# Kernel optimization log

Measured on AMD Instinct MI355X. Metric: run time of the kernel, lower is better.

## Reference

```python
import jax, jax.numpy as jnp
import numpy as np

N_NODES = 100000
N_EDGES = 1600000
N_GRAPHS = 2048
HID = 64
IN_F = 14
N_CLS = 2
EPS = 1e-5


def _gcn_conv(x, row, col, w_edge, W, b, n_nodes):
    # PyG GCNConv with add_self_loops=True, normalize=True.
    xw = x @ W  # [N, out]
    # degree on target nodes, self-loop contributes weight 1
    deg = jnp.zeros((n_nodes,), x.dtype).at[col].add(w_edge) + 1.0
    dinv = deg ** -0.5
    norm = dinv[row] * w_edge * dinv[col]  # [E]
    out = jnp.zeros_like(xw).at[col].add(norm[:, None] * xw[row])
    out = out + (dinv * dinv)[:, None] * xw  # self-loop term
    return out + b


def _bn_relu(x, gamma, beta):
    mean = jnp.mean(x, axis=0)
    var = jnp.var(x, axis=0)  # biased, as PyTorch BN training normalization
    y = gamma * (x - mean) * jax.lax.rsqrt(var + EPS) + beta
    return jax.nn.relu(y)


def setup_inputs() -> dict:
    key = jax.random.key(0)
    ks = jax.random.split(key, 8)
    x = jax.random.normal(ks[0], (N_NODES, IN_F), dtype=jnp.float32)
    edge_index = jax.random.randint(ks[1], (2, N_EDGES), 0, N_NODES, dtype=jnp.int64)
    batch = jnp.sort(jax.random.randint(ks[2], (N_NODES,), 0, N_GRAPHS, dtype=jnp.int64))
    edge_weight = jnp.ones((N_EDGES,), dtype=jnp.float32)
    def lin(k, fi, fo):
        s = 1.0 / np.sqrt(fi)
        kw, kb = jax.random.split(k)
        return (jax.random.uniform(kw, (fi, fo), jnp.float32, -s, s),
                jax.random.uniform(kb, (fo,), jnp.float32, -s, s))
    W1, b1 = lin(ks[3], IN_F, HID)
    W2, b2 = lin(ks[4], HID, HID)
    W3, b3 = lin(ks[5], HID, HID)
    fcW, fcb = lin(ks[6], HID, N_CLS)
    g = jnp.ones((HID,), jnp.float32)
    z = jnp.zeros((HID,), jnp.float32)
    return {
        "x": x, "edge_index": edge_index, "batch": batch, "edge_weight": edge_weight,
        "W1": W1, "b1": b1, "W2": W2, "b2": b2, "W3": W3, "b3": b3,
        "g1": g, "bt1": z, "g2": g, "bt2": z, "g3": g, "bt3": z,
        "fcW": fcW, "fcb": fcb,
    }


def reference(x, edge_index, batch, edge_weight, W1, b1, W2, b2, W3, b3,
              g1, bt1, g2, bt2, g3, bt3, fcW, fcb):
    row, col = edge_index[0], edge_index[1]
    n = x.shape[0]
    h = _bn_relu(_gcn_conv(x, row, col, edge_weight, W1, b1, n), g1, bt1)
    h = _bn_relu(_gcn_conv(h, row, col, edge_weight, W2, b2, n), g2, bt2)
    h = _bn_relu(_gcn_conv(h, row, col, edge_weight, W3, b3, n), g3, bt3)
    node_embs = h  # dropout p=0 is identity
    graph_emb = jax.ops.segment_sum(node_embs, batch, num_segments=N_GRAPHS)
    out = graph_emb @ fcW + fcb
    return (out, node_embs, graph_emb)
```

## Files before the change

### kernel.cpp

```cpp
#include <hip/hip_runtime.h>

#define N_NODES 100000
#define N_EDGES 1600000
#define N_GRAPHS 2048
#define HID 64
#define IN_F 14
#define N_CLS 2
#define EPS 1e-5f

typedef _Float16 half_t;
typedef _Float16 half8 __attribute__((ext_vector_type(8)));
typedef float f32x4 __attribute__((ext_vector_type(4)));

#define GSTRIDE ((size_t)N_NODES * 16)

__global__ __launch_bounds__(256) void hist_rank_kernel(const int* __restrict__ col,
                                                        const float* __restrict__ w,
                                                        unsigned long long* __restrict__ packed,
                                                        int* __restrict__ rank, int E) {
    int stride = gridDim.x * blockDim.x;
    for (int e = blockIdx.x * blockDim.x + threadIdx.x; e < E; e += stride) {
        int c = col[e];
        unsigned int fx = __float2uint_rn(w[e] * 65536.0f);
        unsigned long long old =
            atomicAdd(&packed[c], ((unsigned long long)fx << 32) | 1ull);
        rank[e] = (int)(old & 0xffffffffull);
    }
}

__global__ __launch_bounds__(256) void dinv_from_packed(const unsigned long long* __restrict__ packed,
                                                        float* __restrict__ dinv, int n) {
    int i = blockIdx.x * blockDim.x + threadIdx.x;
    if (i < n) {
        float wsum = (float)(packed[i] >> 32) * (1.0f / 65536.0f);
        dinv[i] = rsqrtf(1.0f + wsum);
    }
}


__global__ __launch_bounds__(256) void blocksum1024_kernel(const unsigned long long* __restrict__ packed,
                                                           int* __restrict__ bsum, int n) {
    __shared__ int ls[256];
    int base = blockIdx.x * 1024 + threadIdx.x * 4;
    int s = 0;
#pragma unroll
    for (int k = 0; k < 4; k++) {
        int i = base + k;
        if (i < n) s += (int)(packed[i] & 0xffffffffull);
    }
    ls[threadIdx.x] = s;
    __syncthreads();
    for (int off = 128; off > 0; off >>= 1) {
        if (threadIdx.x < off) ls[threadIdx.x] += ls[threadIdx.x + off];
        __syncthreads();
    }
    if (threadIdx.x == 0) bsum[blockIdx.x] = ls[0];
}

__global__ __launch_bounds__(512) void topscan_kernel(int* __restrict__ bsum, int nb) {
    __shared__ int ls[512];
    int t = threadIdx.x;
    int v = (t < nb) ? bsum[t] : 0;
    ls[t] = v;
    __syncthreads();
    for (int off = 1; off < 512; off <<= 1) {
        int x = ls[t];
        if (t >= off) x += ls[t - off];
        __syncthreads();
        ls[t] = x;
        __syncthreads();
    }
    if (t < nb) bsum[t] = ls[t] - v;
}

__global__ __launch_bounds__(256) void blockscan1024_kernel(const unsigned long long* __restrict__ packed,
                                                            const int* __restrict__ bsum,
                                                            int* __restrict__ ptr, int n, int E) {
    __shared__ int ls[256];
    int base = blockIdx.x * 1024 + threadIdx.x * 4;
    int c[4];
    int s = 0;
#pragma unroll
    for (int k = 0; k < 4; k++) {
        int i = base + k;
        c[k] = (i < n) ? (int)(packed[i] & 0xffffffffull) : 0;
        s += c[k];
    }
    ls[threadIdx.x] = s;
    __syncthreads();
    for (int off = 1; off < 256; off <<= 1) {
        int x = ls[threadIdx.x];
        if (threadIdx.x >= off) x += ls[threadIdx.x - off];
        __syncthreads();
        ls[threadIdx.x] = x;
        __syncthreads();
    }
    int run = ls[threadIdx.x] - s + bsum[blockIdx.x];
#pragma unroll
    for (int k = 0; k < 4; k++) {
        int i = base + k;
        if (i < n) ptr[i] = run;
        run += c[k];
    }
    if (blockIdx.x == 0 && threadIdx.x == 0) ptr[n] = E;
}

__global__ __launch_bounds__(256) void permute_kernel(const int* __restrict__ row,
                                                      const int* __restrict__ col,
                                                      const float* __restrict__ w,
                                                      const float* __restrict__ dinv,
                                                      const int* __restrict__ ptr,
                                                      const int* __restrict__ rank,
                                                      unsigned int* __restrict__ edges, int E) {
    int stride = gridDim.x * blockDim.x;
    for (int e = blockIdx.x * blockDim.x + threadIdx.x; e < E; e += stride) {
        int r = row[e], c = col[e];
        int pos = ptr[c] + rank[e];
        float nrm = dinv[r] * w[e] * dinv[c];
        unsigned int nb = __float_as_uint(nrm);
        unsigned int n15 = (nb + 0x8000u) >> 16;
        if (n15 > 0x7fffu) n15 = 0x7fffu;
        edges[pos] = ((unsigned int)r << 15) | n15;
    }
}


template <int K>
__global__ __launch_bounds__(256) void gemm_kernel(const float* __restrict__ h,
                                                   const float* __restrict__ W,
                                                   half_t* __restrict__ xw, int n_nodes) {
    int f = threadIdx.x & 63;
    float wcol[K];
#pragma unroll
    for (int k = 0; k < K; k++) wcol[k] = W[k * HID + f];
    half_t* xg = xw + (size_t)(f >> 4) * GSTRIDE + (f & 15);
    int wave = (blockIdx.x * blockDim.x + threadIdx.x) >> 6;
    int nwaves = (gridDim.x * blockDim.x) >> 6;
    for (int n = wave; n < n_nodes; n += nwaves) {
        const float* hr = h + (size_t)n * K;
        float acc = 0.f;
#pragma unroll
        for (int k = 0; k < K; k++) acc += hr[k] * wcol[k];
        xg[(size_t)n * 16] = (half_t)acc;
    }
}

__global__ __launch_bounds__(256) void gemm_bn_mfma_kernel(const float* __restrict__ h,
                                                           const float* __restrict__ W,
                                                           const float* __restrict__ stats,
                                                           const float* __restrict__ gamma,
                                                           const float* __restrict__ beta,
                                                           half_t* __restrict__ xw, int n_nodes) {
    __shared__ float sc_s[HID], sh_s[HID];
    if (threadIdx.x < 64) {
        float mean = stats[threadIdx.x] * (1.0f / N_NODES);
        float var = stats[64 + threadIdx.x] * (1.0f / N_NODES) - mean * mean;
        float sc = gamma[threadIdx.x] * rsqrtf(var + EPS);
        sc_s[threadIdx.x] = sc;
        sh_s[threadIdx.x] = beta[threadIdx.x] - mean * sc;
    }
    __syncthreads();
    int lane = threadIdx.x & 63;
    int col16 = lane & 15;
    int quad = lane >> 4;

    float scA[2][8], shA[2][8];
#pragma unroll
    for (int kh = 0; kh < 2; kh++)
#pragma unroll
        for (int j = 0; j < 8; j++) {
            int k = kh * 32 + quad * 8 + j;
            scA[kh][j] = sc_s[k];
            shA[kh][j] = sh_s[k];
        }

    half8 bfrag[4][2];
#pragma unroll
    for (int t = 0; t < 4; t++)
#pragma unroll
        for (int kh = 0; kh < 2; kh++)
#pragma unroll
            for (int j = 0; j < 8; j++) {
                int k = kh * 32 + quad * 8 + j;
                bfrag[t][kh][j] = (half_t)W[k * HID + t * 16 + col16];
            }

    int wave = (blockIdx.x * blockDim.x + threadIdx.x) >> 6;
    int nwaves = (gridDim.x * blockDim.x) >> 6;
    int ntiles = n_nodes >> 4;
    for (int tIdx = wave; tIdx < ntiles; tIdx += nwaves) {
        int n0 = tIdx << 4;
        const float* hr = h + (size_t)(n0 + col16) * HID + quad * 8;
        half8 afrag[2];
#pragma unroll
        for (int kh = 0; kh < 2; kh++) {
            float4 p0 = *(const float4*)(hr + kh * 32);
            float4 p1 = *(const float4*)(hr + kh * 32 + 4);
            float fv[8] = {p0.x, p0.y, p0.z, p0.w, p1.x, p1.y, p1.z, p1.w};
#pragma unroll
            for (int j = 0; j < 8; j++) {
                float v = fv[j] * scA[kh][j] + shA[kh][j];
                afrag[kh][j] = (half_t)fmaxf(v, 0.f);
            }
        }
        f32x4 acc[4];
#pragma unroll
        for (int t = 0; t < 4; t++) {
            f32x4 z = {0.f, 0.f, 0.f, 0.f};
            acc[t] = __builtin_amdgcn_mfma_f32_16x16x32_f16(afrag[0], bfrag[t][0], z, 0, 0, 0);
            acc[t] = __builtin_amdgcn_mfma_f32_16x16x32_f16(afrag[1], bfrag[t][1], acc[t], 0, 0, 0);
        }
#pragma unroll
        for (int t = 0; t < 4; t++) {
            half_t* xg = xw + (size_t)t * GSTRIDE;
#pragma unroll
            for (int r = 0; r < 4; r++) {
                int rowi = n0 + quad * 4 + r;
                xg[(size_t)rowi * 16 + col16] = (half_t)acc[t][r];
            }
        }
    }
}

__global__ __launch_bounds__(256) void gather_stats_kernel(const int* __restrict__ ptr,
                                                           const unsigned int* __restrict__ edges,
                                                           const half_t* __restrict__ xw,
                                                           const float* __restrict__ dinv,
                                                           const float* __restrict__ b,
                                                           float* __restrict__ h,
                                                           float* __restrict__ stats,
                                                           int n_nodes) {
    int g = (blockIdx.x & 7) >> 1;
    int grank = ((blockIdx.x >> 3) << 1) | (blockIdx.x & 1);
    int lane16 = threadIdx.x & 15;
    int quadLocal = threadIdx.x >> 4;
    int quadId = grank * 16 + quadLocal;
    int nquads = (gridDim.x >> 2) * 16;

    const half_t* xg = xw + (size_t)g * GSTRIDE;
    const char* xgb = (const char*)xg + lane16 * 2;
    int f = g * 16 + lane16;
    float bf = b[f];
    int base = ((threadIdx.x & 63) >> 4) * 16;

    float s = 0.f, s2 = 0.f;
    for (int n = quadId; n < n_nodes; n += nquads) {
        int beg = ptr[n];
        int c = ptr[n + 1] - beg;
        float a0 = 0.f, a1 = 0.f, a2 = 0.f, a3 = 0.f;
        for (int j0 = 0; j0 < c; j0 += 16) {
            int m = c - j0;
            if (m > 16) m = 16;
            int ev = 0;
            if (lane16 < m) ev = (int)edges[beg + j0 + lane16];
            int j = 0;
            for (; j + 4 <= m; j += 4) {
                unsigned int u0 = (unsigned int)__shfl(ev, base + j);
                unsigned int u1 = (unsigned int)__shfl(ev, base + j + 1);
                unsigned int u2 = (unsigned int)__shfl(ev, base + j + 2);
                unsigned int u3 = (unsigned int)__shfl(ev, base + j + 3);
                float w0 = __uint_as_float((u0 & 0x7fffu) << 16);
                float w1 = __uint_as_float((u1 & 0x7fffu) << 16);
                float w2 = __uint_as_float((u2 & 0x7fffu) << 16);
                float w3 = __uint_as_float((u3 & 0x7fffu) << 16);
                float x0 = (float)*(const half_t*)(xgb + ((size_t)(u0 >> 15) << 5));
                float x1 = (float)*(const half_t*)(xgb + ((size_t)(u1 >> 15) << 5));
                float x2 = (float)*(const half_t*)(xgb + ((size_t)(u2 >> 15) << 5));
                float x3 = (float)*(const half_t*)(xgb + ((size_t)(u3 >> 15) << 5));
                a0 += w0 * x0; a1 += w1 * x1; a2 += w2 * x2; a3 += w3 * x3;
            }
            if (j < m) {
                unsigned int u = (unsigned int)__shfl(ev, base + j);
                a1 += __uint_as_float((u & 0x7fffu) << 16) *
                      (float)*(const half_t*)(xgb + ((size_t)(u >> 15) << 5));
            }
            if (j + 1 < m) {
                unsigned int u = (unsigned int)__shfl(ev, base + j + 1);
                a2 += __uint_as_float((u & 0x7fffu) << 16) *
                      (float)*(const half_t*)(xgb + ((size_t)(u >> 15) << 5));
            }
            if (j + 2 < m) {
                unsigned int u = (unsigned int)__shfl(ev, base + j + 2);
                a3 += __uint_as_float((u & 0x7fffu) << 16) *
                      (float)*(const half_t*)(xgb + ((size_t)(u >> 15) << 5));
            }
        }
        float di = dinv[n];
        float v = ((a0 + a1) + (a2 + a3)) + di * di * (float)xg[(size_t)n * 16 + lane16] + bf;
        h[(size_t)n * HID + f] = v;
        s += v;
        s2 += v * v;
    }
    __shared__ float ls[256], ls2[256];
    ls[threadIdx.x] = s;
    ls2[threadIdx.x] = s2;
    __syncthreads();
    if (threadIdx.x < 16) {
        float a = 0.f, aa = 0.f;
#pragma unroll
        for (int k = 0; k < 16; k++) {
            a += ls[k * 16 + threadIdx.x];
            aa += ls2[k * 16 + threadIdx.x];
        }
        atomicAdd(&stats[g * 16 + threadIdx.x], a);
        atomicAdd(&stats[64 + g * 16 + threadIdx.x], aa);
    }
}

__global__ __launch_bounds__(256) void bn_relu_seg_kernel(float* __restrict__ h,
                                                          const float* __restrict__ stats,
                                                          const float* __restrict__ gamma,
                                                          const float* __restrict__ beta,
                                                          const int* __restrict__ batch,
                                                          float* __restrict__ gemb,
                                                          int n_nodes) {
    int g = blockIdx.x * blockDim.x + threadIdx.x;
    int f = g & 63;
    int wave = g >> 6;
    int nwaves = (gridDim.x * blockDim.x) >> 6;
    int chunk = (n_nodes + nwaves - 1) / nwaves;
    int n0 = wave * chunk;
    int n1 = n0 + chunk;
    if (n1 > n_nodes) n1 = n_nodes;
    if (n0 >= n_nodes) return;
    float mean = stats[f] * (1.0f / N_NODES);
    float var = stats[64 + f] * (1.0f / N_NODES) - mean * mean;
    float sc = gamma[f] * rsqrtf(var + EPS);
    float sh = beta[f] - mean * sc;
    int curg = batch[n0];
    float racc = 0.f;
    for (int n = n0; n < n1; n++) {
        int bg = batch[n];
        if (bg != curg) {
            atomicAdd(&gemb[(size_t)curg * HID + f], racc);
            racc = 0.f;
            curg = bg;
        }
        size_t idx = (size_t)n * HID + f;
        float v = h[idx] * sc + sh;
        v = fmaxf(v, 0.f);
        h[idx] = v;
        racc += v;
    }
    atomicAdd(&gemb[(size_t)curg * HID + f], racc);
}

__global__ __launch_bounds__(256) void final_kernel(const float* __restrict__ gemb,
                                                    const float* __restrict__ fcW,
                                                    const float* __restrict__ fcb,
                                                    float* __restrict__ out) {
    int g = blockIdx.x * blockDim.x + threadIdx.x;
    if (g >= N_GRAPHS * N_CLS) return;
    int gr = g >> 1, c = g & 1;
    float acc = fcb[c];
#pragma unroll
    for (int k = 0; k < HID; k++) acc += gemb[gr * HID + k] * fcW[k * N_CLS + c];
    out[g] = acc;
}


extern "C" void kernel_launch(void* const* d_in, const int* in_sizes, int n_in,
                              void* d_out, int out_size, void* d_ws, size_t ws_size,
                              hipStream_t stream) {
    const float* x    = (const float*)d_in[0];
    const int*   ei   = (const int*)d_in[1];
    const int*   batch= (const int*)d_in[2];
    const float* ew   = (const float*)d_in[3];
    const float* W1   = (const float*)d_in[4];
    const float* b1   = (const float*)d_in[5];
    const float* W2   = (const float*)d_in[6];
    const float* b2   = (const float*)d_in[7];
    const float* W3   = (const float*)d_in[8];
    const float* b3   = (const float*)d_in[9];
    const float* g1   = (const float*)d_in[10];
    const float* bt1  = (const float*)d_in[11];
    const float* g2   = (const float*)d_in[12];
    const float* bt2  = (const float*)d_in[13];
    const float* g3   = (const float*)d_in[14];
    const float* bt3  = (const float*)d_in[15];
    const float* fcW  = (const float*)d_in[16];
    const float* fcb  = (const float*)d_in[17];

    const int* row = ei;
    const int* col = ei + N_EDGES;

    float* out_head  = (float*)d_out;
    float* node_embs = out_head + N_GRAPHS * N_CLS;
    float* gemb      = node_embs + (size_t)N_NODES * HID;

    half_t* xwh  = (half_t*)d_ws;
    unsigned int* edges = (unsigned int*)(xwh + (size_t)N_NODES * HID);
    unsigned long long* packed = (unsigned long long*)(edges + N_EDGES);
    float* dinv  = (float*)(packed + N_NODES);
    float* stats = dinv + N_NODES;
    int*   ptr   = (int*)(stats + 128);
    int*   rank  = ptr + N_NODES + 1;
    int*   bsum  = rank + N_EDGES;

    const int B   = 256;
    const int gN  = (N_NODES + B - 1) / B;
    const int NBS = (N_NODES + 1023) / 1024;
    const int gGS = 1024;
    const int gGA = 2048;

    hipMemsetAsync(packed, 0, N_NODES * sizeof(unsigned long long), stream);
    hist_rank_kernel<<<gGS, B, 0, stream>>>(col, ew, packed, rank, N_EDGES);
    dinv_from_packed<<<gN, B, 0, stream>>>(packed, dinv, N_NODES);
    blocksum1024_kernel<<<NBS, B, 0, stream>>>(packed, bsum, N_NODES);
    topscan_kernel<<<1, 512, 0, stream>>>(bsum, NBS);
    blockscan1024_kernel<<<NBS, B, 0, stream>>>(packed, bsum, ptr, N_NODES, N_EDGES);
    permute_kernel<<<gGS, B, 0, stream>>>(row, col, ew, dinv, ptr, rank, edges, N_EDGES);

    float* h = node_embs;

    gemm_kernel<IN_F><<<gGS, B, 0, stream>>>(x, W1, xwh, N_NODES);
    hipMemsetAsync(stats, 0, 128 * sizeof(float), stream);
    gather_stats_kernel<<<gGA, B, 0, stream>>>(ptr, edges, xwh, dinv, b1, h, stats, N_NODES);

    gemm_bn_mfma_kernel<<<gGS, B, 0, stream>>>(h, W2, stats, g1, bt1, xwh, N_NODES);
    hipMemsetAsync(stats, 0, 128 * sizeof(float), stream);
    gather_stats_kernel<<<gGA, B, 0, stream>>>(ptr, edges, xwh, dinv, b2, h, stats, N_NODES);

    gemm_bn_mfma_kernel<<<gGS, B, 0, stream>>>(h, W3, stats, g2, bt2, xwh, N_NODES);
    hipMemsetAsync(stats, 0, 128 * sizeof(float), stream);
    gather_stats_kernel<<<gGA, B, 0, stream>>>(ptr, edges, xwh, dinv, b3, h, stats, N_NODES);

    hipMemsetAsync(gemb, 0, (size_t)N_GRAPHS * HID * sizeof(float), stream);
    bn_relu_seg_kernel<<<gGS, B, 0, stream>>>(h, stats, g3, bt3, batch, gemb, N_NODES);

    final_kernel<<<(N_GRAPHS * N_CLS + B - 1) / B, B, 0, stream>>>(gemb, fcW, fcb, out_head);
}
```

Measured before the change: 493.9 us.

## Replace global-atomic CSR build with two-pass bucketed counting sort

The CSR construction previously used per-edge 64-bit global atomics on per-node counters to get degrees and ranks, followed by a scan and a permute. It is replaced by a two-level radix-style sort: per-block shared-memory histograms over 512-node buckets, a scan, a scatter into bucket order, then a per-bucket kernel that does local counting, prefix sums, dinv computation and final placement. The goal is to avoid heavy global atomic contention and random rank traffic. In exchange it adds extra passes over 8-byte edge records and quantizes edge weights to 13 fractional bits, and it aliases the workspace buffers (EB over xwh, EA over edges). Edge order within a node is now nondeterministic.

New measurement: 440.4 us. 1.12x faster.

```diff
diff --git a/kernel.cpp b/kernel.cpp
--- a/kernel.cpp
+++ b/kernel.cpp
@@ -8,53 +8,41 @@
 #define N_CLS 2
 #define EPS 1e-5f
 
+#define BSHIFT 9
+#define NBUCK 196
+#define ABLOCKS 256
+#define CHUNK (N_EDGES / ABLOCKS)
+
 typedef _Float16 half_t;
 typedef _Float16 half8 __attribute__((ext_vector_type(8)));
 typedef float f32x4 __attribute__((ext_vector_type(4)));
 
 #define GSTRIDE ((size_t)N_NODES * 16)
 
-__global__ __launch_bounds__(256) void hist_rank_kernel(const int* __restrict__ col,
-                                                        const float* __restrict__ w,
-                                                        unsigned long long* __restrict__ packed,
-                                                        int* __restrict__ rank, int E) {
-    int stride = gridDim.x * blockDim.x;
-    for (int e = blockIdx.x * blockDim.x + threadIdx.x; e < E; e += stride) {
-        int c = col[e];
-        unsigned int fx = __float2uint_rn(w[e] * 65536.0f);
-        unsigned long long old =
-            atomicAdd(&packed[c], ((unsigned long long)fx << 32) | 1ull);
-        rank[e] = (int)(old & 0xffffffffull);
-    }
-}
-
-__global__ __launch_bounds__(256) void dinv_from_packed(const unsigned long long* __restrict__ packed,
-                                                        float* __restrict__ dinv, int n) {
-    int i = blockIdx.x * blockDim.x + threadIdx.x;
-    if (i < n) {
-        float wsum = (float)(packed[i] >> 32) * (1.0f / 65536.0f);
-        dinv[i] = rsqrtf(1.0f + wsum);
-    }
-}
-
-
-__global__ __launch_bounds__(256) void blocksum1024_kernel(const unsigned long long* __restrict__ packed,
-                                                           int* __restrict__ bsum, int n) {
+
+__global__ __launch_bounds__(256) void histA_kernel(const int* __restrict__ col,
+                                                    int* __restrict__ histG) {
+    __shared__ int hl[NBUCK];
+    for (int i = threadIdx.x; i < NBUCK; i += 256) hl[i] = 0;
+    __syncthreads();
+    int e0 = blockIdx.x * CHUNK;
+    for (int e = e0 + threadIdx.x; e < e0 + CHUNK; e += 256)
+        atomicAdd(&hl[col[e] >> BSHIFT], 1);
+    __syncthreads();
+    for (int i = threadIdx.x; i < NBUCK; i += 256)
+        histG[i * ABLOCKS + blockIdx.x] = hl[i];
+}
+
+__global__ __launch_bounds__(256) void scanS1_kernel(const int* __restrict__ histG,
+                                                     int* __restrict__ bsumA) {
     __shared__ int ls[256];
-    int base = blockIdx.x * 1024 + threadIdx.x * 4;
-    int s = 0;
-#pragma unroll
-    for (int k = 0; k < 4; k++) {
-        int i = base + k;
-        if (i < n) s += (int)(packed[i] & 0xffffffffull);
-    }
-    ls[threadIdx.x] = s;
+    ls[threadIdx.x] = histG[blockIdx.x * 256 + threadIdx.x];
     __syncthreads();
     for (int off = 128; off > 0; off >>= 1) {
         if (threadIdx.x < off) ls[threadIdx.x] += ls[threadIdx.x + off];
         __syncthreads();
     }
-    if (threadIdx.x == 0) bsum[blockIdx.x] = ls[0];
+    if (threadIdx.x == 0) bsumA[blockIdx.x] = ls[0];
 }
 
 __global__ __launch_bounds__(512) void topscan_kernel(int* __restrict__ bsum, int nb) {
@@ -73,20 +61,13 @@
     if (t < nb) bsum[t] = ls[t] - v;
 }
 
-__global__ __launch_bounds__(256) void blockscan1024_kernel(const unsigned long long* __restrict__ packed,
-                                                            const int* __restrict__ bsum,
-                                                            int* __restrict__ ptr, int n, int E) {
+__global__ __launch_bounds__(256) void scanS3_kernel(int* __restrict__ histG,
+                                                     const int* __restrict__ bsumA,
+                                                     int* __restrict__ ptr) {
     __shared__ int ls[256];
-    int base = blockIdx.x * 1024 + threadIdx.x * 4;
-    int c[4];
-    int s = 0;
-#pragma unroll
-    for (int k = 0; k < 4; k++) {
-        int i = base + k;
-        c[k] = (i < n) ? (int)(packed[i] & 0xffffffffull) : 0;
-        s += c[k];
-    }
-    ls[threadIdx.x] = s;
+    int idx = blockIdx.x * 256 + threadIdx.x;
+    int v = histG[idx];
+    ls[threadIdx.x] = v;
     __syncthreads();
     for (int off = 1; off < 256; off <<= 1) {
         int x = ls[threadIdx.x];
@@ -95,32 +76,92 @@
         ls[threadIdx.x] = x;
         __syncthreads();
     }
-    int run = ls[threadIdx.x] - s + bsum[blockIdx.x];
-#pragma unroll
-    for (int k = 0; k < 4; k++) {
-        int i = base + k;
-        if (i < n) ptr[i] = run;
-        run += c[k];
-    }
-    if (blockIdx.x == 0 && threadIdx.x == 0) ptr[n] = E;
-}
-
-__global__ __launch_bounds__(256) void permute_kernel(const int* __restrict__ row,
-                                                      const int* __restrict__ col,
-                                                      const float* __restrict__ w,
-                                                      const float* __restrict__ dinv,
-                                                      const int* __restrict__ ptr,
-                                                      const int* __restrict__ rank,
-                                                      unsigned int* __restrict__ edges, int E) {
+    histG[idx] = ls[threadIdx.x] - v + bsumA[blockIdx.x];
+    if (blockIdx.x == 0 && threadIdx.x == 0) ptr[N_NODES] = N_EDGES;
+}
+
+__global__ __launch_bounds__(256) void scatterA_kernel(const int* __restrict__ row,
+                                                       const int* __restrict__ col,
+                                                       const float* __restrict__ w,
+                                                       const int* __restrict__ histG,
+                                                       int2* __restrict__ EA) {
+    __shared__ int cur[NBUCK];
+    for (int i = threadIdx.x; i < NBUCK; i += 256)
+        cur[i] = histG[i * ABLOCKS + blockIdx.x];
+    __syncthreads();
+    int e0 = blockIdx.x * CHUNK;
+    for (int e = e0 + threadIdx.x; e < e0 + CHUNK; e += 256) {
+        int c = col[e];
+        int r = row[e];
+        int fx = (int)__float2uint_rn(w[e] * 8192.0f);
+        int pos = atomicAdd(&cur[c >> BSHIFT], 1);
+        EA[pos] = make_int2(r, (fx << 17) | c);
+    }
+}
+
+__global__ __launch_bounds__(256) void bucket_kernel(const int2* __restrict__ EA,
+                                                     const int* __restrict__ bsumA,
+                                                     int2* __restrict__ EB,
+                                                     int* __restrict__ ptr,
+                                                     float* __restrict__ dinv) {
+    __shared__ int hist[512], wsum[512], cur[512];
+    int b = blockIdx.x;
+    int beg = bsumA[b];
+    int end = (b == NBUCK - 1) ? N_EDGES : bsumA[b + 1];
+    int i0 = threadIdx.x, i1 = threadIdx.x + 256;
+    hist[i0] = 0; hist[i1] = 0;
+    wsum[i0] = 0; wsum[i1] = 0;
+    __syncthreads();
+    for (int e = beg + threadIdx.x; e < end; e += 256) {
+        int2 ed = EA[e];
+        int c9 = ed.y & 511;
+        atomicAdd(&hist[c9], 1);
+        atomicAdd(&wsum[c9], (int)((unsigned int)ed.y >> 17));
+    }
+    __syncthreads();
+    int cnt0 = hist[i0], cnt1 = hist[i1];
+    for (int off = 1; off < 512; off <<= 1) {
+        int v0 = hist[i0], v1 = hist[i1];
+        int a0 = (i0 >= off) ? hist[i0 - off] : 0;
+        int a1 = (i1 >= off) ? hist[i1 - off] : 0;
+        __syncthreads();
+        hist[i0] = v0 + a0;
+        hist[i1] = v1 + a1;
+        __syncthreads();
+    }
+    int excl0 = hist[i0] - cnt0, excl1 = hist[i1] - cnt1;
+    cur[i0] = beg + excl0;
+    cur[i1] = beg + excl1;
+    int col0 = (b << BSHIFT) + i0, col1 = (b << BSHIFT) + i1;
+    if (col0 < N_NODES) {
+        ptr[col0] = beg + excl0;
+        dinv[col0] = rsqrtf(1.0f + (float)wsum[i0] * (1.0f / 8192.0f));
+    }
+    if (col1 < N_NODES) {
+        ptr[col1] = beg + excl1;
+        dinv[col1] = rsqrtf(1.0f + (float)wsum[i1] * (1.0f / 8192.0f));
+    }
+    __syncthreads();
+    for (int e = beg + threadIdx.x; e < end; e += 256) {
+        int2 ed = EA[e];
+        int pos = atomicAdd(&cur[ed.y & 511], 1);
+        EB[pos] = ed;
+    }
+}
+
+__global__ __launch_bounds__(256) void finalize_kernel(const int2* __restrict__ EB,
+                                                       const float* __restrict__ dinv,
+                                                       unsigned int* __restrict__ edges, int E) {
     int stride = gridDim.x * blockDim.x;
     for (int e = blockIdx.x * blockDim.x + threadIdx.x; e < E; e += stride) {
-        int r = row[e], c = col[e];
-        int pos = ptr[c] + rank[e];
-        float nrm = dinv[r] * w[e] * dinv[c];
+        int2 ed = EB[e];
+        int c = ed.y & 0x1ffff;
+        float w = (float)((unsigned int)ed.y >> 17) * (1.0f / 8192.0f);
+        float nrm = dinv[ed.x] * w * dinv[c];
         unsigned int nb = __float_as_uint(nrm);
         unsigned int n15 = (nb + 0x8000u) >> 16;
         if (n15 > 0x7fffu) n15 = 0x7fffu;
-        edges[pos] = ((unsigned int)r << 15) | n15;
+        edges[e] = ((unsigned int)ed.x << 15) | n15;
     }
 }
 
@@ -388,28 +429,30 @@
     float* node_embs = out_head + N_GRAPHS * N_CLS;
     float* gemb      = node_embs + (size_t)N_NODES * HID;
 
-    half_t* xwh  = (half_t*)d_ws;
-    unsigned int* edges = (unsigned int*)(xwh + (size_t)N_NODES * HID);
-    unsigned long long* packed = (unsigned long long*)(edges + N_EDGES);
-    float* dinv  = (float*)(packed + N_NODES);
+    char* base = (char*)d_ws;
+    half_t* xwh = (half_t*)base;
+    int2*   EB  = (int2*)base;
+    char* r1 = base + (size_t)N_NODES * HID * 2;
+    int2*   EA  = (int2*)r1;
+    unsigned int* edges = (unsigned int*)r1;
+    char* r2 = r1 + (size_t)N_EDGES * 8;
+    float* dinv  = (float*)r2;
     float* stats = dinv + N_NODES;
     int*   ptr   = (int*)(stats + 128);
-    int*   rank  = ptr + N_NODES + 1;
-    int*   bsum  = rank + N_EDGES;
+    int*   histG = ptr + N_NODES + 1;
+    int*   bsumA = histG + NBUCK * ABLOCKS;
 
     const int B   = 256;
-    const int gN  = (N_NODES + B - 1) / B;
-    const int NBS = (N_NODES + 1023) / 1024;
     const int gGS = 1024;
     const int gGA = 2048;
 
-    hipMemsetAsync(packed, 0, N_NODES * sizeof(unsigned long long), stream);
-    hist_rank_kernel<<<gGS, B, 0, stream>>>(col, ew, packed, rank, N_EDGES);
-    dinv_from_packed<<<gN, B, 0, stream>>>(packed, dinv, N_NODES);
-    blocksum1024_kernel<<<NBS, B, 0, stream>>>(packed, bsum, N_NODES);
-    topscan_kernel<<<1, 512, 0, stream>>>(bsum, NBS);
-    blockscan1024_kernel<<<NBS, B, 0, stream>>>(packed, bsum, ptr, N_NODES, N_EDGES);
-    permute_kernel<<<gGS, B, 0, stream>>>(row, col, ew, dinv, ptr, rank, edges, N_EDGES);
+    histA_kernel<<<ABLOCKS, B, 0, stream>>>(col, histG);
+    scanS1_kernel<<<NBUCK, B, 0, stream>>>(histG, bsumA);
+    topscan_kernel<<<1, 512, 0, stream>>>(bsumA, NBUCK);
+    scanS3_kernel<<<NBUCK, B, 0, stream>>>(histG, bsumA, ptr);
+    scatterA_kernel<<<ABLOCKS, B, 0, stream>>>(row, col, ew, histG, EA);
+    bucket_kernel<<<NBUCK, B, 0, stream>>>(EA, bsumA, EB, ptr, dinv);
+    finalize_kernel<<<gGS, B, 0, stream>>>(EB, dinv, edges, N_EDGES);
 
     float* h = node_embs;
 
```
